# Kernel optimization log

Hardware: AMD Instinct MI355X
Metric: run time of the kernel (lower is better)

## Reference

```python
import jax, jax.numpy as jnp
import numpy as np

N_NODES = 10000
N_EDGES = 320000
D = 256
D_OUT = 256
NUM_REL = 2


def setup_inputs() -> dict:
    key = jax.random.key(0)
    ks = jax.random.split(key, 16)
    s = 1.0 / np.sqrt(D)
    inp = {}
    inp['feat'] = jax.random.normal(ks[0], (N_NODES, D), dtype=jnp.float32)
    inp['src'] = jax.random.randint(ks[1], (N_EDGES,), 0, N_NODES, dtype=jnp.int32)
    inp['dst'] = jax.random.randint(ks[2], (N_EDGES,), 0, N_NODES, dtype=jnp.int32)
    inp['rel'] = jax.random.randint(ks[3], (N_EDGES,), 0, NUM_REL, dtype=jnp.int32)
    # per-relation edgeNN: ONE tied Linear(D, D) applied twice with relu
    inp['W_rel'] = jax.random.normal(ks[4], (NUM_REL, D, D), dtype=jnp.float32) * s
    inp['b_rel'] = jax.random.normal(ks[5], (NUM_REL, D), dtype=jnp.float32) * s
    # LSTM (single step from zero state: W_hh contributes 0, omitted)
    inp['W_ih'] = jax.random.normal(ks[6], (4 * D, D), dtype=jnp.float32) * s
    inp['b_ih'] = jax.random.normal(ks[7], (4 * D,), dtype=jnp.float32) * s
    inp['b_hh'] = jax.random.normal(ks[8], (4 * D,), dtype=jnp.float32) * s
    # global_update MLP: D -> D/2 -> D/2 -> D_OUT
    h = D // 2
    inp['W1'] = jax.random.normal(ks[9], (h, D), dtype=jnp.float32) * s
    inp['b1'] = jax.random.normal(ks[10], (h,), dtype=jnp.float32) * s
    inp['W2'] = jax.random.normal(ks[11], (h, h), dtype=jnp.float32) * (1.0 / np.sqrt(h))
    inp['b2'] = jax.random.normal(ks[12], (h,), dtype=jnp.float32) * (1.0 / np.sqrt(h))
    inp['W3'] = jax.random.normal(ks[13], (D_OUT, h), dtype=jnp.float32) * (1.0 / np.sqrt(h))
    inp['b3'] = jax.random.normal(ks[14], (D_OUT,), dtype=jnp.float32) * (1.0 / np.sqrt(h))
    return inp


def reference(feat, src, dst, rel, W_rel, b_rel, W_ih, b_ih, b_hh,
              W1, b1, W2, b2, W3, b3):
    n_nodes = feat.shape[0]
    # ---- message: per-edge relation-typed tied-weight MLP ----
    S = feat[src]  # [E, D] gather of source features

    def edge_nn(x, W, b):
        h = jax.nn.relu(x @ W.T + b)
        return jax.nn.relu(h @ W.T + b)  # same lin1 applied twice (tied)

    msgs = jnp.zeros_like(S)
    for r in range(W_rel.shape[0]):  # small fixed relation count
        msgs = jnp.where((rel == r)[:, None], edge_nn(S, W_rel[r], b_rel[r]), msgs)

    # ---- reduce: scatter-sum into destination nodes ----
    agg = jax.ops.segment_sum(msgs, dst, num_segments=n_nodes)  # [N, D]

    # ---- apply: per-node single-step LSTM from zero (h0, c0) ----
    gates = agg @ W_ih.T + b_ih + b_hh  # [N, 4D], torch gate order i,f,g,o
    i, f, g, o = jnp.split(gates, 4, axis=-1)
    c = jax.nn.sigmoid(i) * jnp.tanh(g)  # f * c0 = 0
    hn = jax.nn.sigmoid(o) * jnp.tanh(c)  # [N, D]

    # ---- global_update MLP ----
    x = jax.nn.relu(hn @ W1.T + b1)
    x = jax.nn.relu(x @ W2.T + b2)
    return x @ W3.T + b3  # [N, D_OUT]
```

## Files before the change

### kernel.cpp

```cpp
#include <hip/hip_runtime.h>
#include <hip/hip_bf16.h>

#define N_NODES 10000
#define N_EDGES 320000
#define D 256

typedef __attribute__((ext_vector_type(8))) _Float16 f16x8;
typedef __attribute__((ext_vector_type(4))) _Float16 f16x4;
typedef __attribute__((ext_vector_type(4))) float f32x4;

__device__ __forceinline__ void async_copy16(const void* g, void* l) {
  __builtin_amdgcn_global_load_lds(
      (const __attribute__((address_space(1))) unsigned int*)g,
      (__attribute__((address_space(3))) unsigned int*)l, 16, 0, 0);
}

template<int ROWS, int WAVES>
__device__ __forceinline__ void stage_tile(const _Float16* __restrict__ Wb, int k0, int K,
                                           _Float16* Bs, int wave, int lane) {
  const int sr = lane >> 2, ss = lane & 3;
#pragma unroll
  for (int grp = wave; grp < ROWS / 16; grp += WAVES) {
    int r = grp * 16 + sr;
    int gq = ss ^ ((r >> 1) & 3);
    async_copy16(Wb + (size_t)r * K + k0 + gq * 8, Bs + grp * 512);
  }
}
__device__ __forceinline__ f16x8 read_B(const _Float16* Bs, int r, int quad) {
  return *(const f16x8*)(Bs + r * 32 + (quad ^ ((r >> 1) & 3)) * 8);
}

__device__ __forceinline__ float fast_sigmoid(float x) {
  return __builtin_amdgcn_rcpf(1.f + __expf(-x));
}
__device__ __forceinline__ float fast_tanh(float x) {
  float ax = fabsf(x);
  float e = __expf(-2.f * ax);
  float t = (1.f - e) * __builtin_amdgcn_rcpf(1.f + e);
  return copysignf(t, x);
}

__global__ void prep_fill(const int* __restrict__ dst, const int* __restrict__ src,
                          const int* __restrict__ rel,
                          int* __restrict__ cnt, unsigned int* __restrict__ rowoff,
                          const float* __restrict__ W_rel, const float* __restrict__ W_ih,
                          const float* __restrict__ b_ih, const float* __restrict__ b_hh,
                          const float* __restrict__ W1, const float* __restrict__ W2,
                          const float* __restrict__ W3,
                          _Float16* __restrict__ W_relh, _Float16* __restrict__ Wg,
                          float* __restrict__ bg,
                          _Float16* __restrict__ W1h, _Float16* __restrict__ W2h,
                          _Float16* __restrict__ W3h) {
  int i = blockIdx.x * 256 + threadIdx.x;
  if (i < N_EDGES) {
    int v = dst[i];
    int pos = atomicAdd(&cnt[v], 1);
    if (pos < 128)
      rowoff[(v << 7) + pos] = (unsigned int)((rel[i] * N_NODES + src[i]) * D);
    return;
  }
  i -= N_EDGES;
  if (i < 131072) { W_relh[i] = (_Float16)W_rel[i]; return; }
  i -= 131072;
  if (i < 196608) {
    int p = i >> 8, k = i & 255;
    int t = p / 48, rem = p - t * 48;
    int phase = rem >> 4, u = rem & 15;
    int orig = t * 16 + u + (phase == 1 ? 512 : (phase == 2 ? 768 : 0));
    Wg[i] = (_Float16)W_ih[orig * 256 + k]; return;
  }
  i -= 196608;
  if (i < 32768) { W1h[i] = (_Float16)W1[i]; return; }
  i -= 32768;
  if (i < 16384) { W2h[i] = (_Float16)W2[i]; return; }
  i -= 16384;
  if (i < 32768) { W3h[i] = (_Float16)W3[i]; return; }
  i -= 32768;
  if (i < 768) {
    int t = i / 48, rem = i - t * 48;
    int phase = rem >> 4, u = rem & 15;
    int orig = t * 16 + u + (phase == 1 ? 512 : (phase == 2 ? 768 : 0));
    bg[i] = b_ih[orig] + b_hh[orig];
  }
}

__global__ __launch_bounds__(512) void edge_fused(
    const float* __restrict__ feat, const _Float16* __restrict__ W_relh,
    const float* __restrict__ b_rel, _Float16* __restrict__ Mh)
{
  __shared__ _Float16 Hs[64 * 266];
  __shared__ alignas(16) _Float16 Bs[256 * 32];
  const int t = threadIdx.x;
  const int wave = t >> 6, lane = t & 63;
  const int quad = lane >> 4, lrow = lane & 15;
  const int z = blockIdx.y;
  const int m0 = blockIdx.x * 64;
  const _Float16* Wb = W_relh + z * 65536;
  const float* bb = b_rel + z * 256;
  const int wm = (wave >> 2) * 32;
  const int wn = (wave & 3) * 64;

  int ar0 = m0 + wm + lrow;      if (ar0 > N_NODES - 1) ar0 = N_NODES - 1;
  int ar1 = m0 + wm + 16 + lrow; if (ar1 > N_NODES - 1) ar1 = N_NODES - 1;
  const float* fr0 = feat + (size_t)ar0 * 256;
  const float* fr1 = feat + (size_t)ar1 * 256;

  f32x4 acc[2][4];
#pragma unroll
  for (int i = 0; i < 2; ++i)
#pragma unroll
    for (int j = 0; j < 4; ++j) acc[i][j] = (f32x4)0.0f;

#pragma unroll
  for (int kc = 0; kc < 8; ++kc) {
    stage_tile<256, 8>(Wb, kc * 32, 256, Bs, wave, lane);
    float4 u0 = *(const float4*)(fr0 + kc * 32 + quad * 8);
    float4 u1 = *(const float4*)(fr0 + kc * 32 + quad * 8 + 4);
    float4 v0 = *(const float4*)(fr1 + kc * 32 + quad * 8);
    float4 v1 = *(const float4*)(fr1 + kc * 32 + quad * 8 + 4);
    f16x8 af0, af1;
    af0[0] = (_Float16)u0.x; af0[1] = (_Float16)u0.y; af0[2] = (_Float16)u0.z; af0[3] = (_Float16)u0.w;
    af0[4] = (_Float16)u1.x; af0[5] = (_Float16)u1.y; af0[6] = (_Float16)u1.z; af0[7] = (_Float16)u1.w;
    af1[0] = (_Float16)v0.x; af1[1] = (_Float16)v0.y; af1[2] = (_Float16)v0.z; af1[3] = (_Float16)v0.w;
    af1[4] = (_Float16)v1.x; af1[5] = (_Float16)v1.y; af1[6] = (_Float16)v1.z; af1[7] = (_Float16)v1.w;
    __syncthreads();
#pragma unroll
    for (int j = 0; j < 4; ++j) {
      f16x8 bf = read_B(Bs, wn + j * 16 + lrow, quad);
      acc[0][j] = __builtin_amdgcn_mfma_f32_16x16x32_f16(af0, bf, acc[0][j], 0, 0, 0);
      acc[1][j] = __builtin_amdgcn_mfma_f32_16x16x32_f16(af1, bf, acc[1][j], 0, 0, 0);
    }
    __syncthreads();
  }
#pragma unroll
  for (int i = 0; i < 2; ++i) {
    int rb = wm + i * 16 + quad * 4;
#pragma unroll
    for (int j = 0; j < 4; ++j) {
      int col = wn + j * 16 + lrow;
      float bv = bb[col];
#pragma unroll
      for (int reg = 0; reg < 4; ++reg) {
        Hs[(rb + reg) * 266 + col] = (_Float16)fmaxf(acc[i][j][reg] + bv, 0.f);
        acc[i][j][reg] = 0.f;
      }
    }
  }
  __syncthreads();

#pragma unroll
  for (int kc = 0; kc < 8; ++kc) {
    stage_tile<256, 8>(Wb, kc * 32, 256, Bs, wave, lane);
    f16x8 af0 = *(const f16x8*)(Hs + (wm + lrow) * 266 + kc * 32 + quad * 8);
    f16x8 af1 = *(const f16x8*)(Hs + (wm + 16 + lrow) * 266 + kc * 32 + quad * 8);
    __syncthreads();
#pragma unroll
    for (int j = 0; j < 4; ++j) {
      f16x8 bf = read_B(Bs, wn + j * 16 + lrow, quad);
      acc[0][j] = __builtin_amdgcn_mfma_f32_16x16x32_f16(af0, bf, acc[0][j], 0, 0, 0);
      acc[1][j] = __builtin_amdgcn_mfma_f32_16x16x32_f16(af1, bf, acc[1][j], 0, 0, 0);
    }
    __syncthreads();
  }
  _Float16* Mo = Mh + (size_t)z * (N_NODES * D);
#pragma unroll
  for (int i = 0; i < 2; ++i) {
    int rb = m0 + wm + i * 16 + quad * 4;
#pragma unroll
    for (int j = 0; j < 4; ++j) {
      int col = wn + j * 16 + lrow;
      float bv = bb[col];
#pragma unroll
      for (int reg = 0; reg < 4; ++reg) {
        int gm = rb + reg;
        if (gm < N_NODES)
          Mo[(size_t)gm * D + col] = (_Float16)fmaxf(acc[i][j][reg] + bv, 0.f);
      }
    }
  }
}

__global__ __launch_bounds__(256) void agg_kernel(const int* __restrict__ cnt,
                                                  const unsigned int* __restrict__ rowoff,
                                                  const _Float16* __restrict__ Mh,
                                                  _Float16* __restrict__ aggh) {
  __shared__ float part[4][256];
  const int node = blockIdx.x;
  const int wave = threadIdx.x >> 6, lane = threadIdx.x & 63;
  const int base = node << 7;
  const int deg = cnt[node];
  float a0 = 0.f, a1 = 0.f, a2 = 0.f, a3 = 0.f;
  for (int j = wave; j < deg; j += 4) {
    unsigned int off = rowoff[base + j];
    f16x4 v = *(const f16x4*)(Mh + (size_t)off + lane * 4);
    a0 += (float)v[0]; a1 += (float)v[1]; a2 += (float)v[2]; a3 += (float)v[3];
  }
  *(float4*)&part[wave][lane * 4] = make_float4(a0, a1, a2, a3);
  __syncthreads();
  if (wave == 0) {
    float4 p0 = *(const float4*)&part[0][lane * 4];
    float4 p1 = *(const float4*)&part[1][lane * 4];
    float4 p2 = *(const float4*)&part[2][lane * 4];
    float4 p3 = *(const float4*)&part[3][lane * 4];
    f16x4 o;
    o[0] = (_Float16)(p0.x + p1.x + p2.x + p3.x);
    o[1] = (_Float16)(p0.y + p1.y + p2.y + p3.y);
    o[2] = (_Float16)(p0.z + p1.z + p2.z + p3.z);
    o[3] = (_Float16)(p0.w + p1.w + p2.w + p3.w);
    *(f16x4*)(aggh + (size_t)node * D + lane * 4) = o;
  }
}

__global__ __launch_bounds__(256) void tail(
    const _Float16* __restrict__ aggh,
    const _Float16* __restrict__ Wg, const float* __restrict__ bg,
    const _Float16* __restrict__ W1h, const float* __restrict__ b1,
    const _Float16* __restrict__ W2h, const float* __restrict__ b2,
    const _Float16* __restrict__ W3h, const float* __restrict__ b3,
    float* __restrict__ out)
{
  __shared__ alignas(16) _Float16 Ws[768 * 32];
  __shared__ _Float16 Hn[16 * 266];
  __shared__ _Float16 Xs[16 * 138];
  __shared__ _Float16 X2s[16 * 138];
  const int t = threadIdx.x;
  const int wave = t >> 6, lane = t & 63;
  const int quad = lane >> 4, lrow = lane & 15;
  const int r0 = blockIdx.x * 16;

  {
    f16x8 af[8];
#pragma unroll
    for (int kc = 0; kc < 8; ++kc)
      af[kc] = *(const f16x8*)(aggh + (size_t)(r0 + lrow) * 256 + kc * 32 + quad * 8);
    f32x4 acc[12];
#pragma unroll
    for (int j = 0; j < 12; ++j) acc[j] = (f32x4)0.0f;
#pragma unroll
    for (int kc = 0; kc < 8; ++kc) {
      stage_tile<768, 4>(Wg, kc * 32, 256, Ws, wave, lane);
      __syncthreads();
#pragma unroll
      for (int j = 0; j < 12; ++j) {
        f16x8 bf = read_B(Ws, (wave * 12 + j) * 16 + lrow, quad);
        acc[j] = __builtin_amdgcn_mfma_f32_16x16x32_f16(af[kc], bf, acc[j], 0, 0, 0);
      }
      __syncthreads();
    }
#pragma unroll
    for (int p = 0; p < 4; ++p) {
      float bvi = bg[(wave * 12 + 3 * p + 0) * 16 + lrow];
      float bvg = bg[(wave * 12 + 3 * p + 1) * 16 + lrow];
      float bvo = bg[(wave * 12 + 3 * p + 2) * 16 + lrow];
      int dcol = (wave * 4 + p) * 16 + lrow;
#pragma unroll
      for (int reg = 0; reg < 4; ++reg) {
        float vi = acc[3 * p + 0][reg] + bvi;
        float vg = acc[3 * p + 1][reg] + bvg;
        float vo = acc[3 * p + 2][reg] + bvo;
        float c = fast_sigmoid(vi) * fast_tanh(vg);
        Hn[(quad * 4 + reg) * 266 + dcol] = (_Float16)(fast_sigmoid(vo) * fast_tanh(c));
      }
    }
  }
  __syncthreads();

  {
    f16x8 af[8];
#pragma unroll
    for (int kc = 0; kc < 8; ++kc)
      af[kc] = *(const f16x8*)(Hn + lrow * 266 + kc * 32 + quad * 8);
    f32x4 acc[2];
    acc[0] = (f32x4)0.0f; acc[1] = (f32x4)0.0f;
#pragma unroll
    for (int kc = 0; kc < 8; ++kc) {
      stage_tile<128, 4>(W1h, kc * 32, 256, Ws, wave, lane);
      __syncthreads();
#pragma unroll
      for (int j = 0; j < 2; ++j) {
        f16x8 bf = read_B(Ws, wave * 32 + j * 16 + lrow, quad);
        acc[j] = __builtin_amdgcn_mfma_f32_16x16x32_f16(af[kc], bf, acc[j], 0, 0, 0);
      }
      __syncthreads();
    }
#pragma unroll
    for (int j = 0; j < 2; ++j) {
      int col = wave * 32 + j * 16 + lrow;
      float bv = b1[col];
#pragma unroll
      for (int reg = 0; reg < 4; ++reg)
        Xs[(quad * 4 + reg) * 138 + col] = (_Float16)fmaxf(acc[j][reg] + bv, 0.f);
    }
  }
  __syncthreads();

  {
    f16x8 af[4];
#pragma unroll
    for (int kc = 0; kc < 4; ++kc)
      af[kc] = *(const f16x8*)(Xs + lrow * 138 + kc * 32 + quad * 8);
    f32x4 acc[2];
    acc[0] = (f32x4)0.0f; acc[1] = (f32x4)0.0f;
#pragma unroll
    for (int kc = 0; kc < 4; ++kc) {
      stage_tile<128, 4>(W2h, kc * 32, 128, Ws, wave, lane);
      __syncthreads();
#pragma unroll
      for (int j = 0; j < 2; ++j) {
        f16x8 bf = read_B(Ws, wave * 32 + j * 16 + lrow, quad);
        acc[j] = __builtin_amdgcn_mfma_f32_16x16x32_f16(af[kc], bf, acc[j], 0, 0, 0);
      }
      __syncthreads();
    }
#pragma unroll
    for (int j = 0; j < 2; ++j) {
      int col = wave * 32 + j * 16 + lrow;
      float bv = b2[col];
#pragma unroll
      for (int reg = 0; reg < 4; ++reg)
        X2s[(quad * 4 + reg) * 138 + col] = (_Float16)fmaxf(acc[j][reg] + bv, 0.f);
    }
  }
  __syncthreads();

  {
    f16x8 af[4];
#pragma unroll
    for (int kc = 0; kc < 4; ++kc)
      af[kc] = *(const f16x8*)(X2s + lrow * 138 + kc * 32 + quad * 8);
    f32x4 acc[4];
#pragma unroll
    for (int j = 0; j < 4; ++j) acc[j] = (f32x4)0.0f;
#pragma unroll
    for (int kc = 0; kc < 4; ++kc) {
      stage_tile<256, 4>(W3h, kc * 32, 128, Ws, wave, lane);
      __syncthreads();
#pragma unroll
      for (int j = 0; j < 4; ++j) {
        f16x8 bf = read_B(Ws, wave * 64 + j * 16 + lrow, quad);
        acc[j] = __builtin_amdgcn_mfma_f32_16x16x32_f16(af[kc], bf, acc[j], 0, 0, 0);
      }
      __syncthreads();
    }
#pragma unroll
    for (int j = 0; j < 4; ++j) {
      int col = wave * 64 + j * 16 + lrow;
      float bv = b3[col];
#pragma unroll
      for (int reg = 0; reg < 4; ++reg)
        out[(size_t)(r0 + quad * 4 + reg) * 256 + col] = acc[j][reg] + bv;
    }
  }
}

extern "C" void kernel_launch(void* const* d_in, const int* in_sizes, int n_in,
                              void* d_out, int out_size, void* d_ws, size_t ws_size,
                              hipStream_t stream) {
  const float* feat  = (const float*)d_in[0];
  const int* src = (const int*)d_in[1];
  const int* dst = (const int*)d_in[2];
  const int* rel = (const int*)d_in[3];
  const float* W_rel = (const float*)d_in[4];
  const float* b_rel = (const float*)d_in[5];
  const float* W_ih  = (const float*)d_in[6];
  const float* b_ih  = (const float*)d_in[7];
  const float* b_hh  = (const float*)d_in[8];
  const float* W1 = (const float*)d_in[9];
  const float* b1 = (const float*)d_in[10];
  const float* W2 = (const float*)d_in[11];
  const float* b2 = (const float*)d_in[12];
  const float* W3 = (const float*)d_in[13];
  const float* b3 = (const float*)d_in[14];
  float* out = (float*)d_out;

  char* ws = (char*)d_ws;
  _Float16* Mh   = (_Float16*)(ws);
  _Float16* aggh = (_Float16*)(ws + 10240000);
  char* wsb = ws + 15360000;
  _Float16* W_relh = (_Float16*)(wsb);
  _Float16* Wg     = (_Float16*)(wsb + 262144);
  _Float16* W1h    = (_Float16*)(wsb + 655360);
  _Float16* W2h    = (_Float16*)(wsb + 720896);
  _Float16* W3h    = (_Float16*)(wsb + 753664);
  float*    bg     = (float*)(wsb + 819200);
  int*      cnt    = (int*)(wsb + 822272);
  unsigned int* rowoff = (unsigned int*)(wsb + 862272);

  (void)hipMemsetAsync(cnt, 0, N_NODES * sizeof(int), stream);
  prep_fill<<<2853, 256, 0, stream>>>(dst, src, rel, cnt, rowoff,
                                      W_rel, W_ih, b_ih, b_hh, W1, W2, W3,
                                      W_relh, Wg, bg, W1h, W2h, W3h);
  edge_fused<<<dim3(157, 2), 512, 0, stream>>>(feat, W_relh, b_rel, Mh);
  agg_kernel<<<N_NODES, 256, 0, stream>>>(cnt, rowoff, Mh, aggh);
  tail<<<625, 256, 0, stream>>>(aggh, Wg, bg, W1h, b1, W2h, b2, W3h, b3, out);
}
```

Before: 211.6 us.

## Fuse aggregation into tail GEMM and merge bucket fill with edge GEMM

```diff
diff --git a/kernel.cpp b/kernel.cpp
--- a/kernel.cpp
+++ b/kernel.cpp
@@ -40,26 +40,19 @@
   return copysignf(t, x);
 }
 
-__global__ void prep_fill(const int* __restrict__ dst, const int* __restrict__ src,
-                          const int* __restrict__ rel,
-                          int* __restrict__ cnt, unsigned int* __restrict__ rowoff,
-                          const float* __restrict__ W_rel, const float* __restrict__ W_ih,
-                          const float* __restrict__ b_ih, const float* __restrict__ b_hh,
-                          const float* __restrict__ W1, const float* __restrict__ W2,
-                          const float* __restrict__ W3,
-                          _Float16* __restrict__ W_relh, _Float16* __restrict__ Wg,
-                          float* __restrict__ bg,
-                          _Float16* __restrict__ W1h, _Float16* __restrict__ W2h,
-                          _Float16* __restrict__ W3h) {
-  int i = blockIdx.x * 256 + threadIdx.x;
-  if (i < N_EDGES) {
-    int v = dst[i];
-    int pos = atomicAdd(&cnt[v], 1);
-    if (pos < 128)
-      rowoff[(v << 7) + pos] = (unsigned int)((rel[i] * N_NODES + src[i]) * D);
-    return;
-  }
-  i -= N_EDGES;
+__global__ __launch_bounds__(512) void prep_cast(
+    int* __restrict__ cnt,
+    const float* __restrict__ W_rel, const float* __restrict__ W_ih,
+    const float* __restrict__ b_ih, const float* __restrict__ b_hh,
+    const float* __restrict__ W1, const float* __restrict__ W2,
+    const float* __restrict__ W3,
+    _Float16* __restrict__ W_relh, _Float16* __restrict__ Wg,
+    float* __restrict__ bg,
+    _Float16* __restrict__ W1h, _Float16* __restrict__ W2h,
+    _Float16* __restrict__ W3h) {
+  int i = blockIdx.x * 512 + threadIdx.x;
+  if (i < 10240) { if (i < N_NODES) cnt[i] = 0; return; }
+  i -= 10240;
   if (i < 131072) { W_relh[i] = (_Float16)W_rel[i]; return; }
   i -= 131072;
   if (i < 196608) {
@@ -84,17 +77,29 @@
   }
 }
 
-__global__ __launch_bounds__(512) void edge_fused(
+__global__ __launch_bounds__(512) void edge_fill(
     const float* __restrict__ feat, const _Float16* __restrict__ W_relh,
-    const float* __restrict__ b_rel, _Float16* __restrict__ Mh)
+    const float* __restrict__ b_rel, _Float16* __restrict__ Mh,
+    const int* __restrict__ dst, const int* __restrict__ src,
+    const int* __restrict__ rel,
+    int* __restrict__ cnt, unsigned int* __restrict__ rowoff)
 {
   __shared__ _Float16 Hs[64 * 266];
   __shared__ alignas(16) _Float16 Bs[256 * 32];
+  const int b = blockIdx.x;
+  if (b >= 314) {
+    int i = (b - 314) * 512 + threadIdx.x;
+    int v = dst[i];
+    int pos = atomicAdd(&cnt[v], 1);
+    if (pos < 128)
+      rowoff[(v << 7) + pos] = (unsigned int)((rel[i] * N_NODES + src[i]) * D);
+    return;
+  }
   const int t = threadIdx.x;
   const int wave = t >> 6, lane = t & 63;
   const int quad = lane >> 4, lrow = lane & 15;
-  const int z = blockIdx.y;
-  const int m0 = blockIdx.x * 64;
+  const int z = (b >= 157) ? 1 : 0;
+  const int m0 = (b - z * 157) * 64;
   const _Float16* Wb = W_relh + z * 65536;
   const float* bb = b_rel + z * 256;
   const int wm = (wave >> 2) * 32;
@@ -180,39 +185,9 @@
   }
 }
 
-__global__ __launch_bounds__(256) void agg_kernel(const int* __restrict__ cnt,
-                                                  const unsigned int* __restrict__ rowoff,
-                                                  const _Float16* __restrict__ Mh,
-                                                  _Float16* __restrict__ aggh) {
-  __shared__ float part[4][256];
-  const int node = blockIdx.x;
-  const int wave = threadIdx.x >> 6, lane = threadIdx.x & 63;
-  const int base = node << 7;
-  const int deg = cnt[node];
-  float a0 = 0.f, a1 = 0.f, a2 = 0.f, a3 = 0.f;
-  for (int j = wave; j < deg; j += 4) {
-    unsigned int off = rowoff[base + j];
-    f16x4 v = *(const f16x4*)(Mh + (size_t)off + lane * 4);
-    a0 += (float)v[0]; a1 += (float)v[1]; a2 += (float)v[2]; a3 += (float)v[3];
-  }
-  *(float4*)&part[wave][lane * 4] = make_float4(a0, a1, a2, a3);
-  __syncthreads();
-  if (wave == 0) {
-    float4 p0 = *(const float4*)&part[0][lane * 4];
-    float4 p1 = *(const float4*)&part[1][lane * 4];
-    float4 p2 = *(const float4*)&part[2][lane * 4];
-    float4 p3 = *(const float4*)&part[3][lane * 4];
-    f16x4 o;
-    o[0] = (_Float16)(p0.x + p1.x + p2.x + p3.x);
-    o[1] = (_Float16)(p0.y + p1.y + p2.y + p3.y);
-    o[2] = (_Float16)(p0.z + p1.z + p2.z + p3.z);
-    o[3] = (_Float16)(p0.w + p1.w + p2.w + p3.w);
-    *(f16x4*)(aggh + (size_t)node * D + lane * 4) = o;
-  }
-}
-
-__global__ __launch_bounds__(256) void tail(
-    const _Float16* __restrict__ aggh,
+__global__ __launch_bounds__(256) void agg_tail(
+    const int* __restrict__ cnt, const unsigned int* __restrict__ rowoff,
+    const _Float16* __restrict__ Mh,
     const _Float16* __restrict__ Wg, const float* __restrict__ bg,
     const _Float16* __restrict__ W1h, const float* __restrict__ b1,
     const _Float16* __restrict__ W2h, const float* __restrict__ b2,
@@ -220,6 +195,7 @@
     float* __restrict__ out)
 {
   __shared__ alignas(16) _Float16 Ws[768 * 32];
+  __shared__ _Float16 As[16 * 266];
   __shared__ _Float16 Hn[16 * 266];
   __shared__ _Float16 Xs[16 * 138];
   __shared__ _Float16 X2s[16 * 138];
@@ -228,11 +204,30 @@
   const int quad = lane >> 4, lrow = lane & 15;
   const int r0 = blockIdx.x * 16;
 
+#pragma unroll
+  for (int n = 0; n < 4; ++n) {
+    const int row = wave * 4 + n;
+    const int node = r0 + row;
+    int deg = cnt[node]; if (deg > 128) deg = 128;
+    const int base = node << 7;
+    float a0 = 0.f, a1 = 0.f, a2 = 0.f, a3 = 0.f;
+    for (int j = 0; j < deg; ++j) {
+      unsigned int off = rowoff[base + j];
+      f16x4 v = *(const f16x4*)(Mh + (size_t)off + lane * 4);
+      a0 += (float)v[0]; a1 += (float)v[1]; a2 += (float)v[2]; a3 += (float)v[3];
+    }
+    As[row * 266 + lane * 4 + 0] = (_Float16)a0;
+    As[row * 266 + lane * 4 + 1] = (_Float16)a1;
+    As[row * 266 + lane * 4 + 2] = (_Float16)a2;
+    As[row * 266 + lane * 4 + 3] = (_Float16)a3;
+  }
+  __syncthreads();
+
   {
     f16x8 af[8];
 #pragma unroll
     for (int kc = 0; kc < 8; ++kc)
-      af[kc] = *(const f16x8*)(aggh + (size_t)(r0 + lrow) * 256 + kc * 32 + quad * 8);
+      af[kc] = *(const f16x8*)(As + lrow * 266 + kc * 32 + quad * 8);
     f32x4 acc[12];
 #pragma unroll
     for (int j = 0; j < 12; ++j) acc[j] = (f32x4)0.0f;
@@ -375,7 +370,6 @@
 
   char* ws = (char*)d_ws;
   _Float16* Mh   = (_Float16*)(ws);
-  _Float16* aggh = (_Float16*)(ws + 10240000);
   char* wsb = ws + 15360000;
   _Float16* W_relh = (_Float16*)(wsb);
   _Float16* Wg     = (_Float16*)(wsb + 262144);
@@ -386,11 +380,10 @@
   int*      cnt    = (int*)(wsb + 822272);
   unsigned int* rowoff = (unsigned int*)(wsb + 862272);
 
-  (void)hipMemsetAsync(cnt, 0, N_NODES * sizeof(int), stream);
-  prep_fill<<<2853, 256, 0, stream>>>(dst, src, rel, cnt, rowoff,
-                                      W_rel, W_ih, b_ih, b_hh, W1, W2, W3,
-                                      W_relh, Wg, bg, W1h, W2h, W3h);
-  edge_fused<<<dim3(157, 2), 512, 0, stream>>>(feat, W_relh, b_rel, Mh);
-  agg_kernel<<<N_NODES, 256, 0, stream>>>(cnt, rowoff, Mh, aggh);
-  tail<<<625, 256, 0, stream>>>(aggh, Wg, bg, W1h, b1, W2h, b2, W3h, b3, out);
-}
+  prep_cast<<<822, 512, 0, stream>>>(cnt, W_rel, W_ih, b_ih, b_hh, W1, W2, W3,
+                                     W_relh, Wg, bg, W1h, W2h, W3h);
+  edge_fill<<<939, 512, 0, stream>>>(feat, W_relh, b_rel, Mh,
+                                     dst, src, rel, cnt, rowoff);
+  agg_tail<<<625, 256, 0, stream>>>(cnt, rowoff, Mh, Wg, bg,
+                                    W1h, b1, W2h, b2, W3h, b3, out);
+}
```

Measured after the change: 290.0 us. 37.1% more time.
